# Kernel optimization log

Hardware: AMD Instinct MI355X
Metric: run time of the kernel (lower is better)

## Reference

```python
import jax, jax.numpy as jnp
import numpy as np

N = 100000      # nodes
E = 1600000     # edges
F_IN = 64       # num_features
H = 64          # nhid
G = 512         # num graphs in batch
C = 2           # num_classes
BN_EPS = 1e-5


def setup_inputs() -> dict:
    key = jax.random.key(0)
    ks = jax.random.split(key, 8)
    x = jax.random.normal(ks[0], (N, F_IN), jnp.float32)
    edge_index = jax.random.randint(ks[1], (2, E), 0, N, dtype=jnp.int64)
    batch = jnp.sort(jax.random.randint(ks[2], (N,), 0, G, dtype=jnp.int64))
    s = lambda k, shp, fan: (jax.random.normal(k, shp, jnp.float32) / np.sqrt(fan)).astype(jnp.float32)
    W1 = s(ks[3], (F_IN, H), F_IN); b1 = jnp.zeros((H,), jnp.float32)
    W2 = s(ks[4], (H, H), H);       b2 = jnp.zeros((H,), jnp.float32)
    Wg = s(ks[5], (H, 1), H);       bg = jnp.zeros((1,), jnp.float32)
    bn_gamma = jnp.ones((H,), jnp.float32); bn_beta = jnp.zeros((H,), jnp.float32)
    bn_mean = jnp.zeros((H,), jnp.float32); bn_var = jnp.ones((H,), jnp.float32)
    W_lin = s(ks[6], (H, C), H);    b_lin = jnp.zeros((C,), jnp.float32)
    return dict(x=x, edge_index=edge_index, batch=batch,
                W1=W1, b1=b1, W2=W2, b2=b2, Wg=Wg, bg=bg,
                bn_gamma=bn_gamma, bn_beta=bn_beta, bn_mean=bn_mean, bn_var=bn_var,
                W_lin=W_lin, b_lin=b_lin)


def reference(x, edge_index, batch, W1, b1, W2, b2, Wg, bg,
              bn_gamma, bn_beta, bn_mean, bn_var, W_lin, b_lin):
    src, dst = edge_index[0], edge_index[1]
    # GINConv (eps=0): h_i = MLP(x_i + sum_{j->i} x_j)
    agg = jax.ops.segment_sum(x[src], dst, num_segments=N)       # [N, F_IN]
    h = x + agg
    h = jnp.maximum(h @ W1 + b1, 0.0) @ W2 + b2                  # [N, H]
    h = jnp.maximum(h, 0.0)                                      # outer ReLU
    # Attentional aggregation: segment softmax of gate, weighted segment-sum
    gate = (h @ Wg + bg)[:, 0]                                   # [N]
    gmax = jax.ops.segment_max(gate, batch, num_segments=G)      # [G]
    ex = jnp.exp(gate - gmax[batch])                             # [N]
    denom = jax.ops.segment_sum(ex, batch, num_segments=G)       # [G]
    alpha = ex / denom[batch]                                    # [N]
    pooled = jax.ops.segment_sum(alpha[:, None] * h, batch, num_segments=G)  # [G, H]
    # BatchNorm1d in eval mode (running stats); dropout is identity in eval
    norm = (pooled - bn_mean) / jnp.sqrt(bn_var + BN_EPS) * bn_gamma + bn_beta
    logits = norm @ W_lin + b_lin                                # [G, C]
    return jax.nn.log_softmax(logits, axis=-1)
```

## Files before the change

### kernel.cpp

```cpp
#include <hip/hip_runtime.h>
#include <math.h>
#include <float.h>

#define BN_EPS 1e-5f
#define PBLK   8192
#define NBUCKP 832
#define ACAP   4096
#define STCAP  3072

typedef short s16x8 __attribute__((ext_vector_type(8)));
typedef float f32x4 __attribute__((ext_vector_type(4)));

__device__ __forceinline__ unsigned short f2bf(float f) {
    unsigned u = __float_as_uint(f);
    u += 0x7FFFu + ((u >> 16) & 1u);
    return (unsigned short)(u >> 16);
}
__device__ __forceinline__ float bf2f(unsigned short b) {
    return __uint_as_float(((unsigned)b) << 16);
}
__device__ __forceinline__ int vtb(int row, int byteoff) {
    return row * 128 + (byteoff ^ ((row & 7) << 4));
}

__global__ __launch_bounds__(512) void prep_partition(
    const float* __restrict__ x, unsigned short* __restrict__ xb,
    const float* __restrict__ W1, const float* __restrict__ W2,
    unsigned short* __restrict__ w1t, unsigned short* __restrict__ w2t,
    const int* __restrict__ src, const int* __restrict__ dst,
    const int* __restrict__ batch, int* __restrict__ gstart,
    int* __restrict__ bcur0, int* __restrict__ packed2,
    int N, int E, int EB, int G)
{
    __shared__ int hist[NBUCKP], lstart[NBUCKP], goff[NBUCKP], cur[NBUCKP];
    __shared__ int sorted[PBLK];
    __shared__ unsigned short sbkt[PBLK];

    int tid = threadIdx.x;
    int lane = tid & 63;
    int blk = blockIdx.x;

    int n4 = N * 16;
    for (int i = blk * 512 + tid; i < n4; i += gridDim.x * 512) {
        float4 f = *(const float4*)(x + (size_t)i * 4);
        ushort4 o;
        o.x = f2bf(f.x); o.y = f2bf(f.y); o.z = f2bf(f.z); o.w = f2bf(f.w);
        *(ushort4*)(xb + (size_t)i * 4) = o;
    }
    for (int i = blk * 512 + tid; i < N; i += gridDim.x * 512) {
        int bi = batch[i];
        int bp = (i == 0) ? -1 : batch[i - 1];
        for (int g = bp + 1; g <= bi; ++g) gstart[g] = i;
        if (i == N - 1)
            for (int g = bi + 1; g <= G; ++g) gstart[g] = N;
    }
    if (blk == 0)
        for (int idx = tid; idx < 4096; idx += 512)
            w1t[idx] = f2bf(W1[(idx & 63) * 64 + (idx >> 6)]);
    if (blk == 1)
        for (int idx = tid; idx < 4096; idx += 512)
            w2t[idx] = f2bf(W2[(idx & 63) * 64 + (idx >> 6)]);

    if (blk >= EB) return;

    int e0 = blk * PBLK;
    int cnt = E - e0; if (cnt > PBLK) cnt = PBLK; if (cnt < 0) cnt = 0;

    for (int i = tid; i < NBUCKP; i += 512) hist[i] = 0;
    __syncthreads();
    for (int i = tid; i < cnt; i += 512)
        atomicAdd(&hist[dst[e0 + i] >> 7], 1);
    __syncthreads();
    if (tid < 64) {
        int carry = 0;
        #pragma unroll
        for (int c = 0; c < NBUCKP / 64; ++c) {
            int idx = c * 64 + lane;
            int v = hist[idx];
            int xv = v;
            #pragma unroll
            for (int d = 1; d < 64; d <<= 1) {
                int t = __shfl_up(xv, d); if (lane >= d) xv += t;
            }
            lstart[idx] = xv - v + carry;
            carry += __shfl(xv, 63);
        }
    }
    __syncthreads();
    for (int i = tid; i < NBUCKP; i += 512) {
        cur[i] = lstart[i];
        if (hist[i] > 0) goff[i] = atomicAdd(&bcur0[i], hist[i]);
    }
    __syncthreads();
    for (int i = tid; i < cnt; i += 512) {
        int d = dst[e0 + i];
        int s = src[e0 + i];
        int b = d >> 7;
        int p = atomicAdd(&cur[b], 1);
        sorted[p] = ((d & 127) << 17) | s;
        sbkt[p] = (unsigned short)b;
    }
    __syncthreads();
    for (int i = tid; i < cnt; i += 512) {
        int b = sbkt[i];
        packed2[(size_t)b * ACAP + goff[b] + (i - lstart[b])] = sorted[i];
    }
}

__global__ __launch_bounds__(512, 4) void bucket_fused(
    const unsigned short* __restrict__ xb,
    const int* __restrict__ packed2, const int* __restrict__ bcur0,
    const unsigned short* __restrict__ w1t, const unsigned short* __restrict__ w2t,
    const float* __restrict__ b1, const float* __restrict__ b2,
    const float* __restrict__ Wg, const float* __restrict__ bg,
    unsigned short* __restrict__ h_out, float* __restrict__ gate_out, int N)
{
    __shared__ char vt_raw[16384];
    __shared__ int stage[STCAP];
    int* hist = (int*)vt_raw;
    int* cur  = hist + 128;
    int* excl = (int*)(vt_raw + 1024);

    int tid = threadIdx.x;
    int lane = tid & 63;
    int wave = tid >> 6;
    int b = blockIdx.x;
    int node0 = b * 128;
    int ecnt = bcur0[b];
    if (ecnt > ACAP) ecnt = ACAP;
    const int* arena = packed2 + (size_t)b * ACAP;

    if (tid < 128) hist[tid] = 0;
    __syncthreads();
    for (int i = tid; i < ecnt; i += 512)
        atomicAdd(&hist[arena[i] >> 17], 1);
    __syncthreads();

    if (tid < 64) {
        int carry = 0;
        #pragma unroll
        for (int c = 0; c < 2; ++c) {
            int idx = c * 64 + lane;
            int v = hist[idx];
            int xv = v;
            #pragma unroll
            for (int d = 1; d < 64; d <<= 1) {
                int t = __shfl_up(xv, d); if (lane >= d) xv += t;
            }
            excl[idx] = xv - v + carry;
            cur[idx]  = xv - v + carry;
            carry += __shfl(xv, 63);
        }
        if (lane == 0) excl[128] = carry;
    }
    __syncthreads();

    for (int i = tid; i < ecnt; i += 512) {
        int v = arena[i];
        int p = atomicAdd(&cur[v >> 17], 1);
        if (p < STCAP) stage[p] = v & 0x1FFFF;
    }
    __syncthreads();

    int rowbase = wave * 16;
    int exv = excl[rowbase + (lane < 17 ? lane : 16)];
    if (exv > STCAP) exv = STCAP;
    __syncthreads();

    for (int m = 0; m < 16; ++m) {
        int ln = rowbase + m;
        int node = node0 + ln;
        if (node < N) {
            int beg  = __builtin_amdgcn_readlane(exv, m);
            int end_ = __builtin_amdgcn_readlane(exv, m + 1);

            float v0 = bf2f(xb[(unsigned)node * 64u + lane]);
            float v1 = 0.f, v2 = 0.f, v3 = 0.f, v4 = 0.f, v5 = 0.f, v6 = 0.f, v7 = 0.f;

            for (int base = beg; base < end_; base += 64) {
                int eiv = (base + lane < end_) ? stage[base + lane] : 0;
                int cnt = end_ - base; if (cnt > 64) cnt = 64;
                int j = 0;
                for (; j + 16 <= cnt; j += 16) {
                    int s0  = __builtin_amdgcn_readlane(eiv, j + 0);
                    int s1  = __builtin_amdgcn_readlane(eiv, j + 1);
                    int s2  = __builtin_amdgcn_readlane(eiv, j + 2);
                    int s3  = __builtin_amdgcn_readlane(eiv, j + 3);
                    int s4  = __builtin_amdgcn_readlane(eiv, j + 4);
                    int s5  = __builtin_amdgcn_readlane(eiv, j + 5);
                    int s6  = __builtin_amdgcn_readlane(eiv, j + 6);
                    int s7  = __builtin_amdgcn_readlane(eiv, j + 7);
                    int s8  = __builtin_amdgcn_readlane(eiv, j + 8);
                    int s9  = __builtin_amdgcn_readlane(eiv, j + 9);
                    int s10 = __builtin_amdgcn_readlane(eiv, j + 10);
                    int s11 = __builtin_amdgcn_readlane(eiv, j + 11);
                    int s12 = __builtin_amdgcn_readlane(eiv, j + 12);
                    int s13 = __builtin_amdgcn_readlane(eiv, j + 13);
                    int s14 = __builtin_amdgcn_readlane(eiv, j + 14);
                    int s15 = __builtin_amdgcn_readlane(eiv, j + 15);
                    unsigned short t0  = xb[(unsigned)s0  * 64u + lane];
                    unsigned short t1  = xb[(unsigned)s1  * 64u + lane];
                    unsigned short t2  = xb[(unsigned)s2  * 64u + lane];
                    unsigned short t3  = xb[(unsigned)s3  * 64u + lane];
                    unsigned short t4  = xb[(unsigned)s4  * 64u + lane];
                    unsigned short t5  = xb[(unsigned)s5  * 64u + lane];
                    unsigned short t6  = xb[(unsigned)s6  * 64u + lane];
                    unsigned short t7  = xb[(unsigned)s7  * 64u + lane];
                    unsigned short t8  = xb[(unsigned)s8  * 64u + lane];
                    unsigned short t9  = xb[(unsigned)s9  * 64u + lane];
                    unsigned short t10 = xb[(unsigned)s10 * 64u + lane];
                    unsigned short t11 = xb[(unsigned)s11 * 64u + lane];
                    unsigned short t12 = xb[(unsigned)s12 * 64u + lane];
                    unsigned short t13 = xb[(unsigned)s13 * 64u + lane];
                    unsigned short t14 = xb[(unsigned)s14 * 64u + lane];
                    unsigned short t15 = xb[(unsigned)s15 * 64u + lane];
                    v0 += bf2f(t0); v1 += bf2f(t1); v2 += bf2f(t2); v3 += bf2f(t3);
                    v4 += bf2f(t4); v5 += bf2f(t5); v6 += bf2f(t6); v7 += bf2f(t7);
                    v0 += bf2f(t8); v1 += bf2f(t9); v2 += bf2f(t10); v3 += bf2f(t11);
                    v4 += bf2f(t12); v5 += bf2f(t13); v6 += bf2f(t14); v7 += bf2f(t15);
                }
                for (; j + 8 <= cnt; j += 8) {
                    int s0 = __builtin_amdgcn_readlane(eiv, j + 0);
                    int s1 = __builtin_amdgcn_readlane(eiv, j + 1);
                    int s2 = __builtin_amdgcn_readlane(eiv, j + 2);
                    int s3 = __builtin_amdgcn_readlane(eiv, j + 3);
                    int s4 = __builtin_amdgcn_readlane(eiv, j + 4);
                    int s5 = __builtin_amdgcn_readlane(eiv, j + 5);
                    int s6 = __builtin_amdgcn_readlane(eiv, j + 6);
                    int s7 = __builtin_amdgcn_readlane(eiv, j + 7);
                    unsigned short t0 = xb[(unsigned)s0 * 64u + lane];
                    unsigned short t1 = xb[(unsigned)s1 * 64u + lane];
                    unsigned short t2 = xb[(unsigned)s2 * 64u + lane];
                    unsigned short t3 = xb[(unsigned)s3 * 64u + lane];
                    unsigned short t4 = xb[(unsigned)s4 * 64u + lane];
                    unsigned short t5 = xb[(unsigned)s5 * 64u + lane];
                    unsigned short t6 = xb[(unsigned)s6 * 64u + lane];
                    unsigned short t7 = xb[(unsigned)s7 * 64u + lane];
                    v0 += bf2f(t0); v1 += bf2f(t1); v2 += bf2f(t2); v3 += bf2f(t3);
                    v4 += bf2f(t4); v5 += bf2f(t5); v6 += bf2f(t6); v7 += bf2f(t7);
                }
                for (; j + 4 <= cnt; j += 4) {
                    int s0 = __builtin_amdgcn_readlane(eiv, j + 0);
                    int s1 = __builtin_amdgcn_readlane(eiv, j + 1);
                    int s2 = __builtin_amdgcn_readlane(eiv, j + 2);
                    int s3 = __builtin_amdgcn_readlane(eiv, j + 3);
                    unsigned short t0 = xb[(unsigned)s0 * 64u + lane];
                    unsigned short t1 = xb[(unsigned)s1 * 64u + lane];
                    unsigned short t2 = xb[(unsigned)s2 * 64u + lane];
                    unsigned short t3 = xb[(unsigned)s3 * 64u + lane];
                    v4 += bf2f(t0); v5 += bf2f(t1); v6 += bf2f(t2); v7 += bf2f(t3);
                }
                for (; j < cnt; ++j) {
                    int s = __builtin_amdgcn_readlane(eiv, j);
                    v1 += bf2f(xb[(unsigned)s * 64u + lane]);
                }
            }
            float v = ((v0 + v1) + (v2 + v3)) + ((v4 + v5) + (v6 + v7));
            *(unsigned short*)(vt_raw + vtb(ln, lane * 2)) = f2bf(v);
        } else {
            *(unsigned short*)(vt_raw + vtb(ln, lane * 2)) = 0;
        }
    }

    {
        int quad = lane >> 4;
        int col  = lane & 15;

        s16x8 a0 = *(const s16x8*)(vt_raw + vtb(rowbase + col, quad * 16));
        s16x8 a1 = *(const s16x8*)(vt_raw + vtb(rowbase + col, 64 + quad * 16));

        float b1v[4], b2v[4], wgv[4];
        #pragma unroll
        for (int nt = 0; nt < 4; ++nt) {
            b1v[nt] = b1[nt * 16 + col];
            b2v[nt] = b2[nt * 16 + col];
            wgv[nt] = Wg[nt * 16 + col];
        }
        float bgv = bg[0];

        f32x4 acc1[4];
        #pragma unroll
        for (int nt = 0; nt < 4; ++nt) {
            int off = (nt * 16 + col) * 64 + quad * 8;
            s16x8 w0 = *(const s16x8*)(w1t + off);
            s16x8 w1 = *(const s16x8*)(w1t + off + 32);
            f32x4 c = {0.f, 0.f, 0.f, 0.f};
            c = __builtin_amdgcn_mfma_f32_16x16x32_bf16(a0, w0, c, 0, 0, 0);
            c = __builtin_amdgcn_mfma_f32_16x16x32_bf16(a1, w1, c, 0, 0, 0);
            acc1[nt] = c;
        }
        #pragma unroll
        for (int nt = 0; nt < 4; ++nt)
            #pragma unroll
            for (int r = 0; r < 4; ++r) {
                float hv = fmaxf(acc1[nt][r] + b1v[nt], 0.f);
                *(unsigned short*)(vt_raw + vtb(rowbase + quad * 4 + r, (nt * 16 + col) * 2)) = f2bf(hv);
            }

        s16x8 g0 = *(const s16x8*)(vt_raw + vtb(rowbase + col, quad * 16));
        s16x8 g1 = *(const s16x8*)(vt_raw + vtb(rowbase + col, 64 + quad * 16));

        f32x4 acc2[4];
        #pragma unroll
        for (int nt = 0; nt < 4; ++nt) {
            int off = (nt * 16 + col) * 64 + quad * 8;
            s16x8 w0 = *(const s16x8*)(w2t + off);
            s16x8 w1 = *(const s16x8*)(w2t + off + 32);
            f32x4 c = {0.f, 0.f, 0.f, 0.f};
            c = __builtin_amdgcn_mfma_f32_16x16x32_bf16(g0, w0, c, 0, 0, 0);
            c = __builtin_amdgcn_mfma_f32_16x16x32_bf16(g1, w1, c, 0, 0, 0);
            acc2[nt] = c;
        }

        int nbase = node0 + rowbase;
        float gp[4] = {0.f, 0.f, 0.f, 0.f};
        #pragma unroll
        for (int nt = 0; nt < 4; ++nt)
            #pragma unroll
            for (int r = 0; r < 4; ++r) {
                float hv = fmaxf(acc2[nt][r] + b2v[nt], 0.f);
                int node = nbase + quad * 4 + r;
                if (node < N)
                    h_out[(size_t)node * 64 + nt * 16 + col] = f2bf(hv);
                gp[r] = fmaf(hv, wgv[nt], gp[r]);
            }
        #pragma unroll
        for (int r = 0; r < 4; ++r) {
            float t = gp[r];
            t += __shfl_xor(t, 1);
            t += __shfl_xor(t, 2);
            t += __shfl_xor(t, 4);
            t += __shfl_xor(t, 8);
            int node = nbase + quad * 4 + r;
            if (col == 0 && node < N) gate_out[node] = t + bgv;
        }
    }
}

__global__ __launch_bounds__(256) void pool_final(
    const unsigned short* __restrict__ h, const float* __restrict__ gate,
    const int* __restrict__ gstart,
    const float* __restrict__ gamma_, const float* __restrict__ beta_,
    const float* __restrict__ mean_, const float* __restrict__ var_,
    const float* __restrict__ Wl, const float* __restrict__ bl,
    float* __restrict__ out)
{
    int g = blockIdx.x;
    int tid = threadIdx.x;

    int start = gstart[g];
    int end   = gstart[g + 1];

    __shared__ float red[4];
    __shared__ float pool_s[4 * 64];

    int lane = tid & 63;
    int wave = tid >> 6;

    float m = -FLT_MAX;
    for (int i = start + tid; i < end; i += 256) m = fmaxf(m, gate[i]);
    #pragma unroll
    for (int off = 32; off; off >>= 1) m = fmaxf(m, __shfl_xor(m, off));
    if (lane == 0) red[wave] = m;
    __syncthreads();
    m = fmaxf(fmaxf(red[0], red[1]), fmaxf(red[2], red[3]));
    __syncthreads();

    float s = 0.f;
    for (int i = start + tid; i < end; i += 256) s += expf(gate[i] - m);
    #pragma unroll
    for (int off = 32; off; off >>= 1) s += __shfl_xor(s, off);
    if (lane == 0) red[wave] = s;
    __syncthreads();
    s = red[0] + red[1] + red[2] + red[3];

    float a0 = 0.f, a1 = 0.f, a2 = 0.f, a3 = 0.f;
    int i = start + wave;
    for (; i + 12 < end; i += 16) {
        float e0 = expf(gate[i]      - m);
        float e1 = expf(gate[i + 4]  - m);
        float e2 = expf(gate[i + 8]  - m);
        float e3 = expf(gate[i + 12] - m);
        float t0 = bf2f(h[(size_t)(i)      * 64 + lane]);
        float t1 = bf2f(h[(size_t)(i + 4)  * 64 + lane]);
        float t2 = bf2f(h[(size_t)(i + 8)  * 64 + lane]);
        float t3 = bf2f(h[(size_t)(i + 12) * 64 + lane]);
        a0 = fmaf(e0, t0, a0);
        a1 = fmaf(e1, t1, a1);
        a2 = fmaf(e2, t2, a2);
        a3 = fmaf(e3, t3, a3);
    }
    for (; i < end; i += 4) {
        float e = expf(gate[i] - m);
        a0 = fmaf(e, bf2f(h[(size_t)i * 64 + lane]), a0);
    }
    pool_s[wave * 64 + lane] = (a0 + a1) + (a2 + a3);
    __syncthreads();

    if (wave == 0) {
        float p = pool_s[lane] + pool_s[64 + lane] + pool_s[128 + lane] + pool_s[192 + lane];
        p = (end > start) ? (p / s) : 0.f;
        float nrm = (p - mean_[lane]) / sqrtf(var_[lane] + BN_EPS) * gamma_[lane] + beta_[lane];
        float l0 = nrm * Wl[lane * 2 + 0];
        float l1 = nrm * Wl[lane * 2 + 1];
        #pragma unroll
        for (int off = 32; off; off >>= 1) {
            l0 += __shfl_xor(l0, off);
            l1 += __shfl_xor(l1, off);
        }
        if (lane == 0) {
            l0 += bl[0];
            l1 += bl[1];
            float mx = fmaxf(l0, l1);
            float lse = mx + logf(expf(l0 - mx) + expf(l1 - mx));
            out[g * 2 + 0] = l0 - lse;
            out[g * 2 + 1] = l1 - lse;
        }
    }
}

extern "C" void kernel_launch(void* const* d_in, const int* in_sizes, int n_in,
                              void* d_out, int out_size, void* d_ws, size_t ws_size,
                              hipStream_t stream)
{
    const float* x     = (const float*)d_in[0];
    const int*   eidx  = (const int*)d_in[1];
    const int*   batch = (const int*)d_in[2];
    const float* W1    = (const float*)d_in[3];
    const float* b1    = (const float*)d_in[4];
    const float* W2    = (const float*)d_in[5];
    const float* b2    = (const float*)d_in[6];
    const float* Wg    = (const float*)d_in[7];
    const float* bg    = (const float*)d_in[8];
    const float* bng   = (const float*)d_in[9];
    const float* bnb   = (const float*)d_in[10];
    const float* bnm   = (const float*)d_in[11];
    const float* bnv   = (const float*)d_in[12];
    const float* Wl    = (const float*)d_in[13];
    const float* bl    = (const float*)d_in[14];
    float* out = (float*)d_out;

    int N = in_sizes[0] / 64;
    int E = in_sizes[1] / 2;
    int G = out_size / 2;
    int NP = ((N + 63) / 64) * 64;
    int NBUCK = (N + 127) / 128;
    int EB = (E + PBLK - 1) / PBLK;
    int GRID_A = 1024 > EB ? 1024 : EB;

    char* w = (char*)d_ws;
    int* packed2 = (int*)w;                     w += (size_t)NBUCK * ACAP * 4;
    unsigned short* hxb  = (unsigned short*)w;  w += (size_t)NP * 64 * 2;
    float* gate  = (float*)w;                   w += ((size_t)N * 4 + 255) / 256 * 256;
    int* bcur0   = (int*)w;                     w += NBUCKP * 4;
    unsigned short* w1t = (unsigned short*)w;   w += 4096 * 2;
    unsigned short* w2t = (unsigned short*)w;   w += 4096 * 2;
    int* gstart  = (int*)w;                     w += ((size_t)(G + 1) * 4 + 255) / 256 * 256;
    unsigned short* hbuf = (unsigned short*)w;

    const int* src = eidx;
    const int* dst = eidx + E;

    hipMemsetAsync(bcur0, 0, NBUCKP * sizeof(int), stream);

    prep_partition<<<GRID_A, 512, 0, stream>>>(x, hxb, W1, W2, w1t, w2t,
                                               src, dst, batch, gstart,
                                               bcur0, packed2,
                                               N, E, EB, G);

    bucket_fused  <<<NBUCK, 512, 0, stream>>>(hxb, packed2, bcur0, w1t, w2t,
                                              b1, b2, Wg, bg, hbuf, gate, N);

    pool_final    <<<G, 256, 0, stream>>>(hbuf, gate, gstart, bng, bnb, bnm, bnv,
                                          Wl, bl, out);
}
```

Measured before the change: 187.0 us.

## Gather fp32 x directly, drop bf16 pre-conversion, use online softmax in pooling

Removes the pass in prep_partition that converted x to bf16 and wrote it to a workspace buffer, so the edge aggregation gathers fp32 rows of x directly. This saves one full read and write of x, but each random neighbour gather now moves twice as many bytes. The pooling kernel switches to a single-pass online max/sum softmax and goes from 256 to 512 threads per graph. The prep grid shrinks to the number of edge blocks.

Measured after the change: 198.5 us. 6.2% more time.

```diff
diff --git a/kernel.cpp b/kernel.cpp
--- a/kernel.cpp
+++ b/kernel.cpp
@@ -24,7 +24,6 @@
 }
 
 __global__ __launch_bounds__(512) void prep_partition(
-    const float* __restrict__ x, unsigned short* __restrict__ xb,
     const float* __restrict__ W1, const float* __restrict__ W2,
     unsigned short* __restrict__ w1t, unsigned short* __restrict__ w2t,
     const int* __restrict__ src, const int* __restrict__ dst,
@@ -40,13 +39,6 @@
     int lane = tid & 63;
     int blk = blockIdx.x;
 
-    int n4 = N * 16;
-    for (int i = blk * 512 + tid; i < n4; i += gridDim.x * 512) {
-        float4 f = *(const float4*)(x + (size_t)i * 4);
-        ushort4 o;
-        o.x = f2bf(f.x); o.y = f2bf(f.y); o.z = f2bf(f.z); o.w = f2bf(f.w);
-        *(ushort4*)(xb + (size_t)i * 4) = o;
-    }
     for (int i = blk * 512 + tid; i < N; i += gridDim.x * 512) {
         int bi = batch[i];
         int bp = (i == 0) ? -1 : batch[i - 1];
@@ -108,7 +100,7 @@
 }
 
 __global__ __launch_bounds__(512, 4) void bucket_fused(
-    const unsigned short* __restrict__ xb,
+    const float* __restrict__ x,
     const int* __restrict__ packed2, const int* __restrict__ bcur0,
     const unsigned short* __restrict__ w1t, const unsigned short* __restrict__ w2t,
     const float* __restrict__ b1, const float* __restrict__ b2,
@@ -174,7 +166,7 @@
             int beg  = __builtin_amdgcn_readlane(exv, m);
             int end_ = __builtin_amdgcn_readlane(exv, m + 1);
 
-            float v0 = bf2f(xb[(unsigned)node * 64u + lane]);
+            float v0 = x[(unsigned)node * 64u + lane];
             float v1 = 0.f, v2 = 0.f, v3 = 0.f, v4 = 0.f, v5 = 0.f, v6 = 0.f, v7 = 0.f;
 
             for (int base = beg; base < end_; base += 64) {
@@ -198,26 +190,26 @@
                     int s13 = __builtin_amdgcn_readlane(eiv, j + 13);
                     int s14 = __builtin_amdgcn_readlane(eiv, j + 14);
                     int s15 = __builtin_amdgcn_readlane(eiv, j + 15);
-                    unsigned short t0  = xb[(unsigned)s0  * 64u + lane];
-                    unsigned short t1  = xb[(unsigned)s1  * 64u + lane];
-                    unsigned short t2  = xb[(unsigned)s2  * 64u + lane];
-                    unsigned short t3  = xb[(unsigned)s3  * 64u + lane];
-                    unsigned short t4  = xb[(unsigned)s4  * 64u + lane];
-                    unsigned short t5  = xb[(unsigned)s5  * 64u + lane];
-                    unsigned short t6  = xb[(unsigned)s6  * 64u + lane];
-                    unsigned short t7  = xb[(unsigned)s7  * 64u + lane];
-                    unsigned short t8  = xb[(unsigned)s8  * 64u + lane];
-                    unsigned short t9  = xb[(unsigned)s9  * 64u + lane];
-                    unsigned short t10 = xb[(unsigned)s10 * 64u + lane];
-                    unsigned short t11 = xb[(unsigned)s11 * 64u + lane];
-                    unsigned short t12 = xb[(unsigned)s12 * 64u + lane];
-                    unsigned short t13 = xb[(unsigned)s13 * 64u + lane];
-                    unsigned short t14 = xb[(unsigned)s14 * 64u + lane];
-                    unsigned short t15 = xb[(unsigned)s15 * 64u + lane];
-                    v0 += bf2f(t0); v1 += bf2f(t1); v2 += bf2f(t2); v3 += bf2f(t3);
-                    v4 += bf2f(t4); v5 += bf2f(t5); v6 += bf2f(t6); v7 += bf2f(t7);
-                    v0 += bf2f(t8); v1 += bf2f(t9); v2 += bf2f(t10); v3 += bf2f(t11);
-                    v4 += bf2f(t12); v5 += bf2f(t13); v6 += bf2f(t14); v7 += bf2f(t15);
+                    float t0  = x[(unsigned)s0  * 64u + lane];
+                    float t1  = x[(unsigned)s1  * 64u + lane];
+                    float t2  = x[(unsigned)s2  * 64u + lane];
+                    float t3  = x[(unsigned)s3  * 64u + lane];
+                    float t4  = x[(unsigned)s4  * 64u + lane];
+                    float t5  = x[(unsigned)s5  * 64u + lane];
+                    float t6  = x[(unsigned)s6  * 64u + lane];
+                    float t7  = x[(unsigned)s7  * 64u + lane];
+                    float t8  = x[(unsigned)s8  * 64u + lane];
+                    float t9  = x[(unsigned)s9  * 64u + lane];
+                    float t10 = x[(unsigned)s10 * 64u + lane];
+                    float t11 = x[(unsigned)s11 * 64u + lane];
+                    float t12 = x[(unsigned)s12 * 64u + lane];
+                    float t13 = x[(unsigned)s13 * 64u + lane];
+                    float t14 = x[(unsigned)s14 * 64u + lane];
+                    float t15 = x[(unsigned)s15 * 64u + lane];
+                    v0 += t0; v1 += t1; v2 += t2; v3 += t3;
+                    v4 += t4; v5 += t5; v6 += t6; v7 += t7;
+                    v0 += t8; v1 += t9; v2 += t10; v3 += t11;
+                    v4 += t12; v5 += t13; v6 += t14; v7 += t15;
                 }
                 for (; j + 8 <= cnt; j += 8) {
                     int s0 = __builtin_amdgcn_readlane(eiv, j + 0);
@@ -228,31 +220,31 @@
                     int s5 = __builtin_amdgcn_readlane(eiv, j + 5);
                     int s6 = __builtin_amdgcn_readlane(eiv, j + 6);
                     int s7 = __builtin_amdgcn_readlane(eiv, j + 7);
-                    unsigned short t0 = xb[(unsigned)s0 * 64u + lane];
-                    unsigned short t1 = xb[(unsigned)s1 * 64u + lane];
-                    unsigned short t2 = xb[(unsigned)s2 * 64u + lane];
-                    unsigned short t3 = xb[(unsigned)s3 * 64u + lane];
-                    unsigned short t4 = xb[(unsigned)s4 * 64u + lane];
-                    unsigned short t5 = xb[(unsigned)s5 * 64u + lane];
-                    unsigned short t6 = xb[(unsigned)s6 * 64u + lane];
-                    unsigned short t7 = xb[(unsigned)s7 * 64u + lane];
-                    v0 += bf2f(t0); v1 += bf2f(t1); v2 += bf2f(t2); v3 += bf2f(t3);
-                    v4 += bf2f(t4); v5 += bf2f(t5); v6 += bf2f(t6); v7 += bf2f(t7);
+                    float t0 = x[(unsigned)s0 * 64u + lane];
+                    float t1 = x[(unsigned)s1 * 64u + lane];
+                    float t2 = x[(unsigned)s2 * 64u + lane];
+                    float t3 = x[(unsigned)s3 * 64u + lane];
+                    float t4 = x[(unsigned)s4 * 64u + lane];
+                    float t5 = x[(unsigned)s5 * 64u + lane];
+                    float t6 = x[(unsigned)s6 * 64u + lane];
+                    float t7 = x[(unsigned)s7 * 64u + lane];
+                    v0 += t0; v1 += t1; v2 += t2; v3 += t3;
+                    v4 += t4; v5 += t5; v6 += t6; v7 += t7;
                 }
                 for (; j + 4 <= cnt; j += 4) {
                     int s0 = __builtin_amdgcn_readlane(eiv, j + 0);
                     int s1 = __builtin_amdgcn_readlane(eiv, j + 1);
                     int s2 = __builtin_amdgcn_readlane(eiv, j + 2);
                     int s3 = __builtin_amdgcn_readlane(eiv, j + 3);
-                    unsigned short t0 = xb[(unsigned)s0 * 64u + lane];
-                    unsigned short t1 = xb[(unsigned)s1 * 64u + lane];
-                    unsigned short t2 = xb[(unsigned)s2 * 64u + lane];
-                    unsigned short t3 = xb[(unsigned)s3 * 64u + lane];
-                    v4 += bf2f(t0); v5 += bf2f(t1); v6 += bf2f(t2); v7 += bf2f(t3);
+                    float t0 = x[(unsigned)s0 * 64u + lane];
+                    float t1 = x[(unsigned)s1 * 64u + lane];
+                    float t2 = x[(unsigned)s2 * 64u + lane];
+                    float t3 = x[(unsigned)s3 * 64u + lane];
+                    v4 += t0; v5 += t1; v6 += t2; v7 += t3;
                 }
                 for (; j < cnt; ++j) {
                     int s = __builtin_amdgcn_readlane(eiv, j);
-                    v1 += bf2f(xb[(unsigned)s * 64u + lane]);
+                    v1 += x[(unsigned)s * 64u + lane];
                 }
             }
             float v = ((v0 + v1) + (v2 + v3)) + ((v4 + v5) + (v6 + v7));
@@ -337,7 +329,7 @@
     }
 }
 
-__global__ __launch_bounds__(256) void pool_final(
+__global__ __launch_bounds__(512) void pool_final(
     const unsigned short* __restrict__ h, const float* __restrict__ gate,
     const int* __restrict__ gstart,
     const float* __restrict__ gamma_, const float* __restrict__ beta_,
@@ -351,46 +343,55 @@
     int start = gstart[g];
     int end   = gstart[g + 1];
 
-    __shared__ float red[4];
-    __shared__ float pool_s[4 * 64];
+    __shared__ float red_m[8], red_s[8];
+    __shared__ float pool_s[8 * 64];
 
     int lane = tid & 63;
     int wave = tid >> 6;
 
-    float m = -FLT_MAX;
-    for (int i = start + tid; i < end; i += 256) m = fmaxf(m, gate[i]);
+    float m = -FLT_MAX, s = 0.f;
+    for (int i = start + tid; i < end; i += 512) {
+        float gv = gate[i];
+        if (gv > m) { s = s * __expf(m - gv) + 1.f; m = gv; }
+        else        { s += __expf(gv - m); }
+    }
     #pragma unroll
-    for (int off = 32; off; off >>= 1) m = fmaxf(m, __shfl_xor(m, off));
-    if (lane == 0) red[wave] = m;
-    __syncthreads();
-    m = fmaxf(fmaxf(red[0], red[1]), fmaxf(red[2], red[3]));
-    __syncthreads();
-
-    float s = 0.f;
-    for (int i = start + tid; i < end; i += 256) s += expf(gate[i] - m);
-    #pragma unroll
-    for (int off = 32; off; off >>= 1) s += __shfl_xor(s, off);
-    if (lane == 0) red[wave] = s;
-    __syncthreads();
-    s = red[0] + red[1] + red[2] + red[3];
+    for (int off = 32; off; off >>= 1) {
+        float mo = __shfl_xor(m, off);
+        float so = __shfl_xor(s, off);
+        float mn = fmaxf(m, mo);
+        s = s * __expf(m - mn) + so * __expf(mo - mn);
+        m = mn;
+    }
+    if (lane == 0) { red_m[wave] = m; red_s[wave] = s; }
+    __syncthreads();
+    {
+        float mn = red_m[0];
+        #pragma unroll
+        for (int w = 1; w < 8; ++w) mn = fmaxf(mn, red_m[w]);
+        float ss = 0.f;
+        #pragma unroll
+        for (int w = 0; w < 8; ++w) ss += red_s[w] * __expf(red_m[w] - mn);
+        m = mn; s = ss;
+    }
 
     float a0 = 0.f, a1 = 0.f, a2 = 0.f, a3 = 0.f;
     int i = start + wave;
-    for (; i + 12 < end; i += 16) {
+    for (; i + 24 < end; i += 32) {
         float e0 = expf(gate[i]      - m);
-        float e1 = expf(gate[i + 4]  - m);
-        float e2 = expf(gate[i + 8]  - m);
-        float e3 = expf(gate[i + 12] - m);
+        float e1 = expf(gate[i + 8]  - m);
+        float e2 = expf(gate[i + 16] - m);
+        float e3 = expf(gate[i + 24] - m);
         float t0 = bf2f(h[(size_t)(i)      * 64 + lane]);
-        float t1 = bf2f(h[(size_t)(i + 4)  * 64 + lane]);
-        float t2 = bf2f(h[(size_t)(i + 8)  * 64 + lane]);
-        float t3 = bf2f(h[(size_t)(i + 12) * 64 + lane]);
+        float t1 = bf2f(h[(size_t)(i + 8)  * 64 + lane]);
+        float t2 = bf2f(h[(size_t)(i + 16) * 64 + lane]);
+        float t3 = bf2f(h[(size_t)(i + 24) * 64 + lane]);
         a0 = fmaf(e0, t0, a0);
         a1 = fmaf(e1, t1, a1);
         a2 = fmaf(e2, t2, a2);
         a3 = fmaf(e3, t3, a3);
     }
-    for (; i < end; i += 4) {
+    for (; i < end; i += 8) {
         float e = expf(gate[i] - m);
         a0 = fmaf(e, bf2f(h[(size_t)i * 64 + lane]), a0);
     }
@@ -398,7 +399,9 @@
     __syncthreads();
 
     if (wave == 0) {
-        float p = pool_s[lane] + pool_s[64 + lane] + pool_s[128 + lane] + pool_s[192 + lane];
+        float p = 0.f;
+        #pragma unroll
+        for (int w = 0; w < 8; ++w) p += pool_s[w * 64 + lane];
         p = (end > start) ? (p / s) : 0.f;
         float nrm = (p - mean_[lane]) / sqrtf(var_[lane] + BN_EPS) * gamma_[lane] + beta_[lane];
         float l0 = nrm * Wl[lane * 2 + 0];
@@ -443,14 +446,12 @@
     int N = in_sizes[0] / 64;
     int E = in_sizes[1] / 2;
     int G = out_size / 2;
-    int NP = ((N + 63) / 64) * 64;
     int NBUCK = (N + 127) / 128;
     int EB = (E + PBLK - 1) / PBLK;
-    int GRID_A = 1024 > EB ? 1024 : EB;
+    int GRID_A = EB > 2 ? EB : 2;
 
     char* w = (char*)d_ws;
     int* packed2 = (int*)w;                     w += (size_t)NBUCK * ACAP * 4;
-    unsigned short* hxb  = (unsigned short*)w;  w += (size_t)NP * 64 * 2;
     float* gate  = (float*)w;                   w += ((size_t)N * 4 + 255) / 256 * 256;
     int* bcur0   = (int*)w;                     w += NBUCKP * 4;
     unsigned short* w1t = (unsigned short*)w;   w += 4096 * 2;
@@ -463,14 +464,14 @@
 
     hipMemsetAsync(bcur0, 0, NBUCKP * sizeof(int), stream);
 
-    prep_partition<<<GRID_A, 512, 0, stream>>>(x, hxb, W1, W2, w1t, w2t,
+    prep_partition<<<GRID_A, 512, 0, stream>>>(W1, W2, w1t, w2t,
                                                src, dst, batch, gstart,
                                                bcur0, packed2,
                                                N, E, EB, G);
 
-    bucket_fused  <<<NBUCK, 512, 0, stream>>>(hxb, packed2, bcur0, w1t, w2t,
+    bucket_fused  <<<NBUCK, 512, 0, stream>>>(x, packed2, bcur0, w1t, w2t,
                                               b1, b2, Wg, bg, hbuf, gate, N);
 
-    pool_final    <<<G, 256, 0, stream>>>(hbuf, gate, gstart, bng, bnb, bnm, bnv,
+    pool_final    <<<G, 512, 0, stream>>>(hbuf, gate, gstart, bng, bnb, bnm, bnv,
                                           Wl, bl, out);
 }
```
